# Optimization experiments

Hardware: AMD Instinct MI355X
Metric: run time of the kernel (lower is better)

Reference implementation:

```python
import jax, jax.numpy as jnp
import numpy as np

B, Z, Y, X = 4, 32, 512, 512
R = 1
W_OCC, W_OFF, W_FEAT = 0.2, 1.0, 1.0
BIG = 10**9


def _hash_zyx(b, z, y, x):
    return ((b * Z + z) * Y + y) * X + x


def _rand_indices(key, n):
    k1, k2, k3, k4 = jax.random.split(key, 4)
    return jnp.stack([
        jax.random.randint(k1, (n,), 0, B),
        jax.random.randint(k2, (n,), 0, Z),
        jax.random.randint(k3, (n,), 0, Y),
        jax.random.randint(k4, (n,), 0, X),
    ], axis=1).astype(jnp.int32)


def setup_inputs() -> dict:
    key = jax.random.key(0)
    k1, k2, k3, k4, k5 = jax.random.split(key, 5)
    Nr, Nl, C = 200_000, 400_000, 16
    return {
        "pred_feat": jax.random.normal(k1, (Nr, 4), dtype=jnp.float32),
        "pred_occ": jax.random.normal(k2, (Nr, 1), dtype=jnp.float32),
        "lidar_features": jax.random.normal(k3, (Nl, C), dtype=jnp.float32),
        "radar_indices": _rand_indices(k4, Nr),
        "lidar_indices": _rand_indices(k5, Nl),
    }


def _local_match(radar_indices, lidar_indices, lidar_features):
    Nr = radar_indices.shape[0]
    Nl = lidar_indices.shape[0]
    # sorted lidar hash table
    hL = _hash_zyx(lidar_indices[:, 0], lidar_indices[:, 1], lidar_indices[:, 2], lidar_indices[:, 3])
    ordL = jnp.argsort(hL)
    hLs = hL[ordL]
    # K = (2R+1)^3 Chebyshev neighborhood offsets
    rng = jnp.arange(-R, R + 1, dtype=jnp.int32)
    dz, dy, dx = jnp.meshgrid(rng, rng, rng, indexing='ij')
    offs = jnp.stack([dz.reshape(-1), dy.reshape(-1), dx.reshape(-1)], axis=1)  # [K,3]
    K = offs.shape[0]
    b, z, y, x = radar_indices[:, 0], radar_indices[:, 1], radar_indices[:, 2], radar_indices[:, 3]
    zz = jnp.clip(z[:, None] + offs[None, :, 0], 0, Z - 1)  # [Nr,K]
    yy = jnp.clip(y[:, None] + offs[None, :, 1], 0, Y - 1)
    xx = jnp.clip(x[:, None] + offs[None, :, 2], 0, X - 1)
    cand_hash = _hash_zyx(b[:, None], zz, yy, xx).reshape(Nr * K)
    pos = jnp.searchsorted(hLs, cand_hash)
    pos_c = jnp.minimum(pos, Nl - 1)
    hit = ((pos < Nl) & (hLs[pos_c] == cand_hash)).reshape(Nr, K)
    dL1 = jnp.abs(offs).sum(axis=1)  # [K]
    dL1_masked = jnp.where(hit, dL1[None, :], BIG)  # [Nr,K]
    best_k = jnp.argmin(dL1_masked, axis=1)  # [Nr]
    rows = jnp.arange(Nr)
    matched = dL1_masked[rows, best_k] < BIG
    pos_best = pos.reshape(Nr, K)[rows, best_k]
    lidar_row = ordL[jnp.minimum(pos_best, Nl - 1)]
    gt_feat = jnp.where(matched[:, None], lidar_features[lidar_row], 0.0)
    dzz = (zz[rows, best_k] - z).astype(jnp.float32)
    dyy = (yy[rows, best_k] - y).astype(jnp.float32)
    dxx = (xx[rows, best_k] - x).astype(jnp.float32)
    gt_offsets = jnp.stack([dzz, dyy, dxx], axis=1)  # [Nr,3]
    return matched, gt_offsets, gt_feat


def reference(pred_feat, pred_occ, lidar_features, radar_indices, lidar_indices):
    matched, gt_d, gt_f = _local_match(radar_indices, lidar_indices, lidar_features)
    # local_match is @torch.no_grad in the original
    matched = jax.lax.stop_gradient(matched)
    gt_d = jax.lax.stop_gradient(gt_d)
    gt_f = jax.lax.stop_gradient(gt_f)
    occ_logits = pred_occ[:, 0]
    t = matched.astype(jnp.float32)
    # BCEWithLogits (mean): softplus(l) - l*t
    occ_loss = jnp.mean(jax.nn.softplus(occ_logits) - occ_logits * t)
    m = t  # [Nr] float mask
    cnt = jnp.sum(m)
    # smooth L1 (beta=1) over matched rows, mean over matched elements
    d = pred_feat[:, :3] - gt_d
    ad = jnp.abs(d)
    sl1 = jnp.where(ad < 1.0, 0.5 * d * d, ad - 0.5)
    off_loss = jnp.sum(sl1 * m[:, None]) / jnp.maximum(cnt * 3.0, 1.0)
    feat_loss = jnp.sum(jnp.abs(pred_feat[:, 3] - gt_f[:, 0]) * m) / jnp.maximum(cnt, 1.0)
    return W_OCC * occ_loss + W_OFF * off_loss + W_FEAT * feat_loss
```

## Files before the change

kernel.cpp:

```cpp
#include <hip/hip_runtime.h>
#include <cstdint>

static constexpr int Z_ = 32, Y_ = 512, X_ = 512;
static constexpr int ROW_WORDS = X_ / 32;
static constexpr size_t NVOX = 4ull * Z_ * Y_ * X_;
static constexpr size_t BITMAP_WORDS = NVOX / 32;
static constexpr size_t BITMAP_BYTES = BITMAP_WORDS * 4;
static constexpr size_t BITMAP_OFF = 65536;
static constexpr size_t RECORDS_OFF = BITMAP_OFF + BITMAP_BYTES;
static constexpr uint32_t REC_SENTINEL = 0xFFFFFFFFu;


__global__ __launch_bounds__(256) void init_preset(
        const int* __restrict__ radar_idx, int Nr,
        uint4* __restrict__ bitmap_v4, uint32_t n_bm4,
        uint32_t* __restrict__ records,
        uint32_t* __restrict__ counter) {
    uint32_t t = blockIdx.x * blockDim.x + threadIdx.x;
    uint32_t stride = gridDim.x * blockDim.x;
    if (t == 0) *counter = 0;
    const uint4 z = make_uint4(0u, 0u, 0u, 0u);
    for (uint32_t i = t; i < n_bm4; i += stride) bitmap_v4[i] = z;
    for (uint32_t i = t; i < (uint32_t)Nr; i += stride) {
        int4 ri = reinterpret_cast<const int4*>(radar_idx)[i];
        uint32_t key = (uint32_t)(((ri.x * Z_ + ri.y) * Y_ + ri.z) * X_ + ri.w);
        __builtin_nontemporal_store(REC_SENTINEL, &records[key]);
    }
}

__global__ void radar_bits(const int* __restrict__ radar_idx, int Nr,
                           uint32_t* __restrict__ bitmap) {
    int i = blockIdx.x * blockDim.x + threadIdx.x;
    if (i >= Nr) return;
    int4 ri = reinterpret_cast<const int4*>(radar_idx)[i];
    uint32_t key = (uint32_t)(((ri.x * Z_ + ri.y) * Y_ + ri.z) * X_ + ri.w);
    atomicOr(&bitmap[key >> 5], 1u << (key & 31));
}

__global__ __launch_bounds__(256) void lidar_pass(
        const int* __restrict__ lidar_idx, int Nl,
        const uint32_t* __restrict__ bitmap,
        uint32_t* __restrict__ records) {
    int i = blockIdx.x * blockDim.x + threadIdx.x;
    if (i >= Nl) return;
    int4 li = reinterpret_cast<const int4*>(lidar_idx)[i];
    const int b = li.x, z = li.y, y = li.z, x = li.w;

    const int xm1 = max(x - 1, 0);
    const int w0  = xm1 >> 5;
    const int w1  = min(w0 + 1, ROW_WORDS - 1);
    const int base = w0 << 5;

    uint32_t mask = 0;
    #pragma unroll
    for (int dz = -1; dz <= 1; ++dz) {
        int zz = z + dz;
        if (zz < 0 || zz >= Z_) continue;
        #pragma unroll
        for (int dy = -1; dy <= 1; ++dy) {
            int yy = y + dy;
            if (yy < 0 || yy >= Y_) continue;
            uint32_t rw = (uint32_t)((b * Z_ + zz) * Y_ + yy) * ROW_WORDS;
            uint64_t win = (uint64_t)bitmap[rw + w0] |
                           ((uint64_t)bitmap[rw + w1] << 32);
            #pragma unroll
            for (int dx = -1; dx <= 1; ++dx) {
                int xx = x + dx;
                if (xx < 0 || xx >= X_) continue;
                int m = (dz + 1) * 9 + (dy + 1) * 3 + (dx + 1);
                mask |= (uint32_t)((win >> (xx - base)) & 1ull) << m;
            }
        }
    }

    while (mask) {
        int m = __builtin_ctz(mask);
        mask &= mask - 1;
        int mdz = m / 9 - 1, mr = m % 9;
        int mdy = mr / 3 - 1, mdx = mr % 3 - 1;
        uint32_t vkey = (uint32_t)(((b * Z_ + (z + mdz)) * Y_ + (y + mdy)) * X_ + (x + mdx));
        uint32_t dl1 = (uint32_t)(abs(mdz) + abs(mdy) + abs(mdx));
        uint32_t k   = (uint32_t)(26 - m);
        uint32_t packed = (dl1 << 24) | (k << 19) | (uint32_t)i;
        atomicMin(&records[vkey], packed);
    }
}

__global__ __launch_bounds__(256) void loss_final(
        const float* __restrict__ pred_feat,
        const float* __restrict__ pred_occ,
        const float* __restrict__ lidar_feat,
        const int* __restrict__ radar_idx,
        const uint32_t* __restrict__ records,
        int Nr, int nblocks,
        float4* __restrict__ partials,
        uint32_t* __restrict__ counter,
        float* __restrict__ out) {
    float occ_a = 0.f, off_a = 0.f, feat_a = 0.f, cnt_a = 0.f;
    int r = blockIdx.x * blockDim.x + threadIdx.x;
    if (r < Nr) {
        int4 ri = reinterpret_cast<const int4*>(radar_idx)[r];
        uint32_t key = (uint32_t)(((ri.x * Z_ + ri.y) * Y_ + ri.z) * X_ + ri.w);
        uint32_t rec = records[key];

        float o = pred_occ[r];
        float sp = fmaxf(o, 0.f) + log1pf(expf(-fabsf(o)));
        bool matched = (rec != REC_SENTINEL);
        occ_a = sp - (matched ? o : 0.f);

        if (matched) {
            cnt_a = 1.f;
            int wk  = (int)((rec >> 19) & 31u);
            int row = (int)(rec & 0x7FFFFu);
            int wdz = wk / 9 - 1, wr = wk % 9;
            int wdy = wr / 3 - 1, wdx = wr % 3 - 1;
            float4 pf = reinterpret_cast<const float4*>(pred_feat)[r];
            float p[3]  = { pf.x, pf.y, pf.z };
            float gt[3] = { (float)wdz, (float)wdy, (float)wdx };
            #pragma unroll
            for (int j = 0; j < 3; ++j) {
                float dd = p[j] - gt[j];
                float ad = fabsf(dd);
                off_a += (ad < 1.f) ? 0.5f * dd * dd : ad - 0.5f;
            }
            feat_a = fabsf(pf.w - lidar_feat[16 * row]);
        }
    }

    #pragma unroll
    for (int o = 32; o >= 1; o >>= 1) {
        occ_a  += __shfl_xor(occ_a,  o, 64);
        off_a  += __shfl_xor(off_a,  o, 64);
        feat_a += __shfl_xor(feat_a, o, 64);
        cnt_a  += __shfl_xor(cnt_a,  o, 64);
    }
    __shared__ float red[4][4];
    __shared__ bool last;
    int wid = threadIdx.x >> 6;
    if ((threadIdx.x & 63) == 0) {
        red[wid][0] = occ_a; red[wid][1] = off_a;
        red[wid][2] = feat_a; red[wid][3] = cnt_a;
    }
    __syncthreads();
    if (threadIdx.x == 0) {
        float s0 = 0.f, s1 = 0.f, s2 = 0.f, s3 = 0.f;
        #pragma unroll
        for (int w = 0; w < 4; ++w) {
            s0 += red[w][0]; s1 += red[w][1]; s2 += red[w][2]; s3 += red[w][3];
        }
        partials[blockIdx.x] = make_float4(s0, s1, s2, s3);
        __threadfence();
        uint32_t prev = atomicAdd(counter, 1u);
        last = (prev == (uint32_t)(nblocks - 1));
    }
    __syncthreads();
    if (last) {
        __threadfence();
        float t0 = 0.f, t1 = 0.f, t2 = 0.f, t3 = 0.f;
        for (int i = threadIdx.x; i < nblocks; i += 256) {
            const float* p = reinterpret_cast<const float*>(&partials[i]);
            t0 += __hip_atomic_load(p + 0, __ATOMIC_RELAXED, __HIP_MEMORY_SCOPE_AGENT);
            t1 += __hip_atomic_load(p + 1, __ATOMIC_RELAXED, __HIP_MEMORY_SCOPE_AGENT);
            t2 += __hip_atomic_load(p + 2, __ATOMIC_RELAXED, __HIP_MEMORY_SCOPE_AGENT);
            t3 += __hip_atomic_load(p + 3, __ATOMIC_RELAXED, __HIP_MEMORY_SCOPE_AGENT);
        }
        #pragma unroll
        for (int o = 32; o >= 1; o >>= 1) {
            t0 += __shfl_xor(t0, o, 64);
            t1 += __shfl_xor(t1, o, 64);
            t2 += __shfl_xor(t2, o, 64);
            t3 += __shfl_xor(t3, o, 64);
        }
        __syncthreads();
        if ((threadIdx.x & 63) == 0) {
            red[wid][0] = t0; red[wid][1] = t1;
            red[wid][2] = t2; red[wid][3] = t3;
        }
        __syncthreads();
        if (threadIdx.x == 0) {
            float s0 = 0.f, s1 = 0.f, s2 = 0.f, s3 = 0.f;
            #pragma unroll
            for (int w = 0; w < 4; ++w) {
                s0 += red[w][0]; s1 += red[w][1]; s2 += red[w][2]; s3 += red[w][3];
            }
            float occ  = s0 / (float)Nr;
            float cnt  = s3;
            float offl = s1 / fmaxf(cnt * 3.f, 1.f);
            float feat = s2 / fmaxf(cnt, 1.f);
            out[0] = 0.2f * occ + offl + feat;
        }
    }
}

extern "C" void kernel_launch(void* const* d_in, const int* in_sizes, int n_in,
                              void* d_out, int out_size, void* d_ws, size_t ws_size,
                              hipStream_t stream) {
    const float* pred_feat  = (const float*)d_in[0];
    const float* pred_occ   = (const float*)d_in[1];
    const float* lidar_feat = (const float*)d_in[2];
    const int*   radar_idx  = (const int*)d_in[3];
    const int*   lidar_idx  = (const int*)d_in[4];
    int Nr = in_sizes[1];
    int Nl = in_sizes[2] / 16;

    uint32_t* counter  = (uint32_t*)d_ws;
    float4*   partials = (float4*)((char*)d_ws + 64);
    uint32_t* bitmap   = (uint32_t*)((char*)d_ws + BITMAP_OFF);
    uint32_t* records  = (uint32_t*)((char*)d_ws + RECORDS_OFF);

    const uint32_t n_bm4 = (uint32_t)(BITMAP_BYTES / 16);
    const int nblocks = (Nr + 255) / 256;

    hipLaunchKernelGGL(init_preset, dim3(1024), dim3(256), 0, stream,
                       radar_idx, Nr, (uint4*)bitmap, n_bm4, records, counter);
    hipLaunchKernelGGL(radar_bits, dim3(nblocks), dim3(256), 0, stream,
                       radar_idx, Nr, bitmap);
    hipLaunchKernelGGL(lidar_pass, dim3((Nl + 255) / 256), dim3(256), 0, stream,
                       lidar_idx, Nl, bitmap, records);
    hipLaunchKernelGGL(loss_final, dim3(nblocks), dim3(256), 0, stream,
                       pred_feat, pred_occ, lidar_feat, radar_idx, records,
                       Nr, nblocks, partials, counter, (float*)d_out);
}
```

Measured before the change: 73.12 us.

## Replace sparse voxel record table with bitmap-rank compacted record array

```diff
diff --git a/kernel.cpp b/kernel.cpp
--- a/kernel.cpp
+++ b/kernel.cpp
@@ -6,26 +6,25 @@
 static constexpr size_t NVOX = 4ull * Z_ * Y_ * X_;
 static constexpr size_t BITMAP_WORDS = NVOX / 32;
 static constexpr size_t BITMAP_BYTES = BITMAP_WORDS * 4;
-static constexpr size_t BITMAP_OFF = 65536;
-static constexpr size_t RECORDS_OFF = BITMAP_OFF + BITMAP_BYTES;
+static constexpr int SCAN_BLOCKS = (int)(BITMAP_WORDS / 256);
 static constexpr uint32_t REC_SENTINEL = 0xFFFFFFFFu;
 
-
-__global__ __launch_bounds__(256) void init_preset(
-        const int* __restrict__ radar_idx, int Nr,
+static constexpr size_t OFF_BITMAP  = 65536;
+static constexpr size_t OFF_OFFSETS = OFF_BITMAP + BITMAP_BYTES;
+static constexpr size_t OFF_BSUMS   = OFF_OFFSETS + BITMAP_BYTES;
+static constexpr size_t OFF_COMPACT = OFF_BSUMS + 65536;
+
+__global__ __launch_bounds__(256) void init_kernel(
         uint4* __restrict__ bitmap_v4, uint32_t n_bm4,
-        uint32_t* __restrict__ records,
+        uint4* __restrict__ compact_v4, uint32_t n_cp4,
         uint32_t* __restrict__ counter) {
     uint32_t t = blockIdx.x * blockDim.x + threadIdx.x;
     uint32_t stride = gridDim.x * blockDim.x;
     if (t == 0) *counter = 0;
     const uint4 z = make_uint4(0u, 0u, 0u, 0u);
+    const uint4 f = make_uint4(~0u, ~0u, ~0u, ~0u);
     for (uint32_t i = t; i < n_bm4; i += stride) bitmap_v4[i] = z;
-    for (uint32_t i = t; i < (uint32_t)Nr; i += stride) {
-        int4 ri = reinterpret_cast<const int4*>(radar_idx)[i];
-        uint32_t key = (uint32_t)(((ri.x * Z_ + ri.y) * Y_ + ri.z) * X_ + ri.w);
-        __builtin_nontemporal_store(REC_SENTINEL, &records[key]);
-    }
+    for (uint32_t i = t; i < n_cp4; i += stride) compact_v4[i] = f;
 }
 
 __global__ void radar_bits(const int* __restrict__ radar_idx, int Nr,
@@ -37,10 +36,59 @@
     atomicOr(&bitmap[key >> 5], 1u << (key & 31));
 }
 
+__global__ __launch_bounds__(256) void scan_sums(
+        const uint32_t* __restrict__ bitmap, uint32_t* __restrict__ blockSums) {
+    int t = threadIdx.x;
+    uint32_t pc = __popc(bitmap[blockIdx.x * 256 + t]);
+    __shared__ uint32_t s[256];
+    s[t] = pc;
+    __syncthreads();
+    #pragma unroll
+    for (int off = 128; off >= 1; off >>= 1) {
+        if (t < off) s[t] += s[t + off];
+        __syncthreads();
+    }
+    if (t == 0) blockSums[blockIdx.x] = s[0];
+}
+
+__global__ __launch_bounds__(256) void scan_offsets(
+        const uint32_t* __restrict__ bitmap,
+        const uint32_t* __restrict__ blockSums,
+        uint32_t* __restrict__ offsets) {
+    int b = blockIdx.x, t = threadIdx.x;
+    uint32_t loc = 0;
+    for (int i = t; i < b; i += 256) loc += blockSums[i];
+    __shared__ uint32_t s[256];
+    __shared__ uint32_t base_s;
+    s[t] = loc;
+    __syncthreads();
+    #pragma unroll
+    for (int off = 128; off >= 1; off >>= 1) {
+        if (t < off) s[t] += s[t + off];
+        __syncthreads();
+    }
+    if (t == 0) base_s = s[0];
+    __syncthreads();
+    uint32_t base = base_s;
+    uint32_t w = (uint32_t)b * 256 + t;
+    uint32_t pc = __popc(bitmap[w]);
+    s[t] = pc;
+    __syncthreads();
+    #pragma unroll
+    for (int off = 1; off < 256; off <<= 1) {
+        uint32_t v = (t >= off) ? s[t - off] : 0u;
+        __syncthreads();
+        s[t] += v;
+        __syncthreads();
+    }
+    offsets[w] = base + s[t] - pc;
+}
+
 __global__ __launch_bounds__(256) void lidar_pass(
         const int* __restrict__ lidar_idx, int Nl,
         const uint32_t* __restrict__ bitmap,
-        uint32_t* __restrict__ records) {
+        const uint32_t* __restrict__ offsets,
+        uint32_t* __restrict__ compact) {
     int i = blockIdx.x * blockDim.x + threadIdx.x;
     if (i >= Nl) return;
     int4 li = reinterpret_cast<const int4*>(lidar_idx)[i];
@@ -52,6 +100,7 @@
     const int base = w0 << 5;
 
     uint32_t mask = 0;
+    uint32_t lo[3][3], hi[3][3];
     #pragma unroll
     for (int dz = -1; dz <= 1; ++dz) {
         int zz = z + dz;
@@ -61,8 +110,11 @@
             int yy = y + dy;
             if (yy < 0 || yy >= Y_) continue;
             uint32_t rw = (uint32_t)((b * Z_ + zz) * Y_ + yy) * ROW_WORDS;
-            uint64_t win = (uint64_t)bitmap[rw + w0] |
-                           ((uint64_t)bitmap[rw + w1] << 32);
+            uint32_t a = bitmap[rw + w0];
+            uint32_t c = bitmap[rw + w1];
+            lo[dz + 1][dy + 1] = a;
+            hi[dz + 1][dy + 1] = c;
+            uint64_t win = (uint64_t)a | ((uint64_t)c << 32);
             #pragma unroll
             for (int dx = -1; dx <= 1; ++dx) {
                 int xx = x + dx;
@@ -78,11 +130,17 @@
         mask &= mask - 1;
         int mdz = m / 9 - 1, mr = m % 9;
         int mdy = mr / 3 - 1, mdx = mr % 3 - 1;
-        uint32_t vkey = (uint32_t)(((b * Z_ + (z + mdz)) * Y_ + (y + mdy)) * X_ + (x + mdx));
+        int zz = z + mdz, yy = y + mdy, xx = x + mdx;
+        uint32_t rw = (uint32_t)((b * Z_ + zz) * Y_ + yy) * ROW_WORDS;
+        int wi = xx >> 5;
+        uint32_t word = (wi == w0) ? lo[mdz + 1][mdy + 1] : hi[mdz + 1][mdy + 1];
+        uint32_t widx = rw + (uint32_t)wi;
+        uint32_t below = word & ((1u << (xx & 31)) - 1u);
+        uint32_t rank = offsets[widx] + __popc(below);
         uint32_t dl1 = (uint32_t)(abs(mdz) + abs(mdy) + abs(mdx));
         uint32_t k   = (uint32_t)(26 - m);
         uint32_t packed = (dl1 << 24) | (k << 19) | (uint32_t)i;
-        atomicMin(&records[vkey], packed);
+        atomicMin(&compact[rank], packed);
     }
 }
 
@@ -91,7 +149,9 @@
         const float* __restrict__ pred_occ,
         const float* __restrict__ lidar_feat,
         const int* __restrict__ radar_idx,
-        const uint32_t* __restrict__ records,
+        const uint32_t* __restrict__ bitmap,
+        const uint32_t* __restrict__ offsets,
+        const uint32_t* __restrict__ compact,
         int Nr, int nblocks,
         float4* __restrict__ partials,
         uint32_t* __restrict__ counter,
@@ -101,7 +161,10 @@
     if (r < Nr) {
         int4 ri = reinterpret_cast<const int4*>(radar_idx)[r];
         uint32_t key = (uint32_t)(((ri.x * Z_ + ri.y) * Y_ + ri.z) * X_ + ri.w);
-        uint32_t rec = records[key];
+        uint32_t widx = key >> 5;
+        uint32_t word = bitmap[widx];
+        uint32_t rank = offsets[widx] + __popc(word & ((1u << (key & 31)) - 1u));
+        uint32_t rec  = compact[rank];
 
         float o = pred_occ[r];
         float sp = fmaxf(o, 0.f) + log1pf(expf(-fabsf(o)));
@@ -203,21 +266,29 @@
     int Nr = in_sizes[1];
     int Nl = in_sizes[2] / 16;
 
-    uint32_t* counter  = (uint32_t*)d_ws;
-    float4*   partials = (float4*)((char*)d_ws + 64);
-    uint32_t* bitmap   = (uint32_t*)((char*)d_ws + BITMAP_OFF);
-    uint32_t* records  = (uint32_t*)((char*)d_ws + RECORDS_OFF);
+    uint32_t* counter   = (uint32_t*)d_ws;
+    float4*   partials  = (float4*)((char*)d_ws + 64);
+    uint32_t* bitmap    = (uint32_t*)((char*)d_ws + OFF_BITMAP);
+    uint32_t* offsets   = (uint32_t*)((char*)d_ws + OFF_OFFSETS);
+    uint32_t* blockSums = (uint32_t*)((char*)d_ws + OFF_BSUMS);
+    uint32_t* compact   = (uint32_t*)((char*)d_ws + OFF_COMPACT);
 
     const uint32_t n_bm4 = (uint32_t)(BITMAP_BYTES / 16);
+    const uint32_t n_cp4 = (uint32_t)((4ull * Nr + 15) / 16);
     const int nblocks = (Nr + 255) / 256;
 
-    hipLaunchKernelGGL(init_preset, dim3(1024), dim3(256), 0, stream,
-                       radar_idx, Nr, (uint4*)bitmap, n_bm4, records, counter);
+    hipLaunchKernelGGL(init_kernel, dim3(1024), dim3(256), 0, stream,
+                       (uint4*)bitmap, n_bm4, (uint4*)compact, n_cp4, counter);
     hipLaunchKernelGGL(radar_bits, dim3(nblocks), dim3(256), 0, stream,
                        radar_idx, Nr, bitmap);
+    hipLaunchKernelGGL(scan_sums, dim3(SCAN_BLOCKS), dim3(256), 0, stream,
+                       bitmap, blockSums);
+    hipLaunchKernelGGL(scan_offsets, dim3(SCAN_BLOCKS), dim3(256), 0, stream,
+                       bitmap, blockSums, offsets);
     hipLaunchKernelGGL(lidar_pass, dim3((Nl + 255) / 256), dim3(256), 0, stream,
-                       lidar_idx, Nl, bitmap, records);
+                       lidar_idx, Nl, bitmap, offsets, compact);
     hipLaunchKernelGGL(loss_final, dim3(nblocks), dim3(256), 0, stream,
-                       pred_feat, pred_occ, lidar_feat, radar_idx, records,
-                       Nr, nblocks, partials, counter, (float*)d_out);
-}
+                       pred_feat, pred_occ, lidar_feat, radar_idx,
+                       bitmap, offsets, compact, Nr, nblocks,
+                       partials, counter, (float*)d_out);
+}
```

Result: slower. 93.60 us (+28.0%).
